# Kernel tuning notes

Hardware: AMD Instinct MI355X
Metric: run time of the kernel (lower is better)

Reference implementation:

```python
import jax, jax.numpy as jnp
import numpy as np

N = 100000   # nodes
E = 200000   # edges
G = 2000     # graphs
D = 300      # emb_dim
L = 5        # layers
FEAT = 512
MAX_DEGREE = 4
EPS = 1e-5


def setup_inputs() -> dict:
    key = jax.random.key(0)
    ks = jax.random.split(key, 24)
    atom_vocab = jnp.array([119, 3, 11, 9, 7, 4, 6, 2, 2])
    bond_vocab = jnp.array([4, 3, 2])  # keep type < 4 so self-loop type 4 is distinct
    x = jax.random.randint(ks[0], (N, 9), 0, 1 << 30) % atom_vocab
    edge_index = jax.random.randint(ks[1], (2, E), 0, N)
    edge_attr = jax.random.randint(ks[2], (E, 3), 0, 1 << 30) % bond_vocab
    edge_distance = jax.random.uniform(ks[3], (E,), dtype=jnp.float32) * 4.0
    batch = jnp.sort(jax.random.randint(ks[4], (N,), 0, G))
    nrm = lambda k, s, sc: (jax.random.normal(k, s, dtype=jnp.float32) * sc)
    return {
        "x": x, "edge_index": edge_index, "edge_attr": edge_attr,
        "edge_distance": edge_distance, "batch": batch,
        "atom_emb": nrm(ks[5], (9, 119, D), 0.1),
        "att_vec": nrm(ks[6], (D,), 1.0),
        "out_lin_w": nrm(ks[7], (D, D), 0.05), "out_lin_b": jnp.zeros((D,)),
        "g_means": jax.random.uniform(ks[8], (D,), minval=2.0, maxval=3.0),
        "g_stds": jax.random.uniform(ks[9], (D,), minval=1.0, maxval=1.5),
        "scale_param": jnp.full((MAX_DEGREE, D), np.log(0.1), dtype=jnp.float32),
        "edge_emb": nrm(ks[10], (L, 3, 5, D), 0.1),
        "mlp_w1": nrm(ks[11], (L, D, 2 * D), 0.05), "mlp_b1": jnp.zeros((L, 2 * D)),
        "mlp_w2": nrm(ks[12], (L, 2 * D, D), 0.05), "mlp_b2": jnp.zeros((L, D)),
        "bn_gamma": jnp.ones((L, D)), "bn_beta": jnp.zeros((L, D)),
        "feat_w": nrm(ks[13], (D, FEAT), 0.05), "feat_b": jnp.zeros((FEAT,)),
        "ol_w1": nrm(ks[14], (FEAT, FEAT), 0.05), "ol_b1": jnp.zeros((FEAT,)),
        "ol_w2": nrm(ks[15], (FEAT, FEAT // 2), 0.05), "ol_b2": jnp.zeros((FEAT // 2,)),
    }


def reference(x, edge_index, edge_attr, edge_distance, batch,
              atom_emb, att_vec, out_lin_w, out_lin_b, g_means, g_stds, scale_param,
              edge_emb, mlp_w1, mlp_b1, mlp_w2, mlp_b2, bn_gamma, bn_beta,
              feat_w, feat_b, ol_w1, ol_b1, ol_w2, ol_b2):
    src, dst = edge_index[0], edge_index[1]
    # node degree from incoming edges, clamped as in the torch code
    counts = jax.ops.segment_sum(jnp.ones((E,), jnp.int32), dst, num_segments=N)
    node_degree = jnp.clip(counts - 1, 0, MAX_DEGREE - 1)
    # GaussianLayer on edge distances -> [E, D]
    std = jnp.abs(g_stds) + 0.01
    a = (2.0 * 3.14159) ** 0.5
    z = (edge_distance[:, None] - g_means[None, :]) / std[None, :]
    g = jnp.exp(-0.5 * z * z) / (a * std[None, :])
    h_in = jax.ops.segment_sum(g, dst, num_segments=N)          # [N, D]
    h_in = jnp.exp(scale_param)[node_degree] * h_in             # ScaleDegreeLayer
    # AtomEncoderAttention: [N, 9, D] embeddings fused by softmax attention
    embs = atom_emb[jnp.arange(9)[None, :], x]                  # [N, 9, D]
    scores = jnp.einsum('nfd,d->nf', embs, att_vec)
    w = jax.nn.softmax(scores, axis=1)
    fused = jnp.einsum('nfd,nf->nd', embs, w)
    h = fused @ out_lin_w + out_lin_b + h_in
    # self-loop augmented edges (same for every layer)
    loop = jnp.arange(N)
    src_a = jnp.concatenate([src, loop])
    dst_a = jnp.concatenate([dst, loop])
    loop_attr = jnp.tile(jnp.array([[4, 0, 0]], edge_attr.dtype), (N, 1))
    attr_a = jnp.concatenate([edge_attr, loop_attr], axis=0)    # [E+N, 3]
    for l in range(L):
        e = (edge_emb[l, 0][attr_a[:, 0]] + edge_emb[l, 1][attr_a[:, 1]]
             + edge_emb[l, 2][attr_a[:, 2]])                     # [E+N, D]
        msg = h[src_a] + e
        agg = jax.ops.segment_sum(msg, dst_a, num_segments=N)
        h = jax.nn.relu(agg @ mlp_w1[l] + mlp_b1[l]) @ mlp_w2[l] + mlp_b2[l]
        mu = h.mean(axis=0)
        var = jnp.mean((h - mu) ** 2, axis=0)
        h = bn_gamma[l] * (h - mu) * jax.lax.rsqrt(var + EPS) + bn_beta[l]
        if l < L - 1:
            h = jax.nn.relu(h)
    # global mean pool
    sums = jax.ops.segment_sum(h, batch, num_segments=G)
    cnt = jax.ops.segment_sum(jnp.ones((N,), h.dtype), batch, num_segments=G)
    hg = sums / jnp.maximum(cnt, 1.0)[:, None]
    h_feat = hg @ feat_w + feat_b                                # [G, 512]
    out = jax.nn.relu(h_feat @ ol_w1 + ol_b1) @ ol_w2 + ol_b2    # [G, 256]
    return (h_feat, out)
```

## Files before the change

### kernel.cpp

```cpp
#include <hip/hip_runtime.h>
#include <hip/hip_bf16.h>


#define NN   100000
#define EE   200000
#define GG   2000
#define DD   300
#define D2   600
#define LL   5
#define FEATN 512
#define OUT2 256
#define ROWS_PER 256
#define RPB  48
#define MLP_LDS (RPB * 632 * 2)

typedef __hip_bfloat16 bf16;
typedef short vec8s __attribute__((ext_vector_type(8)));
typedef short vec4s __attribute__((ext_vector_type(4)));
typedef float vec4f __attribute__((ext_vector_type(4)));

__device__ __forceinline__ short f2bs(float v) {
    bf16 h = __float2bfloat16(v);
    return __builtin_bit_cast(short, h);
}
__device__ __forceinline__ float bs2f(short s) {
    unsigned u = ((unsigned)(unsigned short)s) << 16;
    return __builtin_bit_cast(float, u);
}

__global__ void k_pack(const float* __restrict__ src, short* __restrict__ dst,
                       int Ksrc, int Nsrc, int KT, int NPAD)
{
    int idx = blockIdx.x * 256 + threadIdx.x;
    int total = KT * NPAD * 32;
    if (idx >= total) return;
    int col = idx % NPAD;
    int tmp = idx / NPAD;
    int kk  = tmp % 32;
    int kt  = tmp / 32;
    int k = kt * 32 + kk;
    short v = 0;
    if (k < Ksrc && col < Nsrc) v = f2bs(src[(size_t)k * Nsrc + col]);
    dst[((size_t)kt * NPAD + col) * 32 + kk] = v;
}

__global__ void k_etab(const float* __restrict__ edge_emb, float* __restrict__ E)
{
    int i = blockIdx.x * 256 + threadIdx.x;
    if (i >= LL * 25 * DD) return;
    int d = i % DD;
    int t = i / DD;
    int c = t % 25;
    int l = t / 25;
    int a0 = (c == 24) ? 4 : (c / 6);
    int a1 = (c == 24) ? 0 : ((c % 6) / 2);
    int a2 = (c == 24) ? 0 : (c % 2);
    const float* e0 = edge_emb + (size_t)((l * 3 + 0) * 5) * DD;
    const float* e1 = edge_emb + (size_t)((l * 3 + 1) * 5) * DD;
    const float* e2 = edge_emb + (size_t)((l * 3 + 2) * 5) * DD;
    E[i] = e0[a0 * DD + d] + e1[a1 * DD + d] + e2[a2 * DD + d];
}

__global__ void k_repack(int* __restrict__ eidx, const int* __restrict__ src,
                         const int* __restrict__ attr)
{
    int i = blockIdx.x * 256 + threadIdx.x;
    if (i >= EE) return;
    int e = eidx[i];
    int c = attr[e * 3] * 6 + attr[e * 3 + 1] * 2 + attr[e * 3 + 2];
    eidx[i] = src[e] | (c << 17);
}

__global__ __launch_bounds__(512, 4) void k_mlp2(
    const short* __restrict__ Qb, const short* __restrict__ W1P,
    const float* __restrict__ b1, const short* __restrict__ W2P,
    const float* __restrict__ b2, void* __restrict__ Pout, int f16out,
    float* __restrict__ RS)
{
    extern __shared__ __align__(16) char smem_c[];
    short* Apan = (short*)smem_c;
    short (*Hl)[632] = (short(*)[632])smem_c;

    const int t = threadIdx.x;
    const int wv = t >> 6, lane = t & 63;
    const int m = lane & 15, quad = lane >> 4;
    const int rb = (int)blockIdx.x * RPB;
    const int rep = ((int)blockIdx.x & 31) * 600;

    {
        const short* qbase = Qb + (size_t)rb * 320;
#pragma unroll
        for (int i = 0; i < 4; i++) {
            int j = i * 8 + wv;
            if (j < 30) {
                int c   = j * 64 + lane;
                int c8  = c >> 3;
                int row = c8 / 5;
                int ch  = (c8 - row * 5) * 8 + (lane & 7);
                const short* src = qbase + (size_t)row * 320
                                 + (size_t)((ch ^ (row & 7)) * 8);
                __builtin_amdgcn_global_load_lds(
                    (const __attribute__((address_space(1))) unsigned int*)src,
                    (__attribute__((address_space(3))) unsigned int*)(smem_c + j * 1024),
                    16, 0, 0);
            }
        }
    }

    const int ql   = quad ^ (m & 3);
    const int eh   = (m >> 2) & 1;
    const int abE  = m * 320 + ql * 8 + eh * 32;
    const int abO  = m * 320 + ql * 8 + (1 - eh) * 32;

    vec4f acc1[3][5];
#pragma unroll
    for (int g = 0; g < 3; g++)
#pragma unroll
        for (int cf = 0; cf < 5; cf++) acc1[g][cf] = (vec4f)0.f;

    const short* w1b = W1P + ((size_t)(wv * 80 + m) * 32) + quad * 8;
    vec8s bcur[5], bnxt[5];
#pragma unroll
    for (int cf = 0; cf < 5; cf++) bcur[cf] = *(const vec8s*)(w1b + cf * 512);

    __syncthreads();

#pragma unroll
    for (int kt = 0; kt < 10; kt++) {
        if (kt < 9) {
            const short* wn = w1b + (size_t)(kt + 1) * 20480;
#pragma unroll
            for (int cf = 0; cf < 5; cf++) bnxt[cf] = *(const vec8s*)(wn + cf * 512);
        }
        const int base = (kt & 1) ? abO : abE;
        const int koff = (kt & ~1) * 32;
        vec8s af[3];
#pragma unroll
        for (int g = 0; g < 3; g++)
            af[g] = *(const vec8s*)(Apan + base + koff + g * 5120);
        __builtin_amdgcn_s_setprio(1);
#pragma unroll
        for (int cf = 0; cf < 5; cf++)
#pragma unroll
            for (int g = 0; g < 3; g++)
                acc1[g][cf] = __builtin_amdgcn_mfma_f32_16x16x32_bf16(
                    bcur[cf], af[g], acc1[g][cf], 0, 0, 0);
        __builtin_amdgcn_s_setprio(0);
#pragma unroll
        for (int cf = 0; cf < 5; cf++) bcur[cf] = bnxt[cf];
    }

    const short* w2b = W2P + ((size_t)(wv * 48 + m) * 32) + quad * 8;
    vec8s b2f[2][3];
#pragma unroll
    for (int cf = 0; cf < 3; cf++) {
        b2f[0][cf] = *(const vec8s*)(w2b + cf * 512);
        b2f[1][cf] = *(const vec8s*)(w2b + 12288 + cf * 512);
    }

    __syncthreads();

#pragma unroll
    for (int g = 0; g < 3; g++) {
#pragma unroll
        for (int cf = 0; cf < 5; cf++) {
            const int col0 = wv * 80 + cf * 16 + quad * 4;
            if (col0 < 600) {
                vec4f bv = *(const vec4f*)(b1 + col0);
                vec4s o;
#pragma unroll
                for (int r = 0; r < 4; r++)
                    o[r] = f2bs(fmaxf(acc1[g][cf][r] + bv[r], 0.f));
                *(vec4s*)&Hl[g * 16 + m][col0] = o;
            } else if (col0 < 608) {
                *(vec4s*)&Hl[g * 16 + m][col0] = (vec4s)0;
            }
        }
    }
    __syncthreads();

    {
        vec4f acc2[3][3];
#pragma unroll
        for (int g = 0; g < 3; g++)
#pragma unroll
            for (int cf = 0; cf < 3; cf++) acc2[g][cf] = (vec4f)0.f;

#pragma unroll
        for (int kt = 0; kt < 19; kt++) {
            vec8s ha[3];
#pragma unroll
            for (int g = 0; g < 3; g++)
                ha[g] = *(const vec8s*)&Hl[g * 16 + m][kt * 32 + quad * 8];
            __builtin_amdgcn_s_setprio(1);
#pragma unroll
            for (int cf = 0; cf < 3; cf++)
#pragma unroll
                for (int g = 0; g < 3; g++)
                    acc2[g][cf] = __builtin_amdgcn_mfma_f32_16x16x32_bf16(
                        ha[g], b2f[kt & 1][cf], acc2[g][cf], 0, 0, 0);
            __builtin_amdgcn_s_setprio(0);
            if (kt < 17) {
                const short* wn = w2b + (size_t)(kt + 2) * 12288;
#pragma unroll
                for (int cf = 0; cf < 3; cf++)
                    b2f[kt & 1][cf] = *(const vec8s*)(wn + cf * 512);
            }
        }

#pragma unroll
        for (int cf = 0; cf < 3; cf++) {
            int gc = wv * 48 + cf * 16 + m;
            bool ok = (gc < DD);
            float bv = ok ? b2[gc] : 0.f;
            float s = 0.f, q = 0.f;
#pragma unroll
            for (int g = 0; g < 3; g++) {
#pragma unroll
                for (int reg = 0; reg < 4; reg++) {
                    int row = rb + g * 16 + quad * 4 + reg;
                    bool vr = row < NN;
                    float v = acc2[g][cf][reg] + bv;
                    if (ok && vr) {
                        if (f16out)
                            ((short*)Pout)[(size_t)row * 300 + gc] = f2bs(v);
                        else
                            ((float*)Pout)[(size_t)row * DD + gc] = v;
                    }
                    if (vr) { s += v; q += v * v; }
                }
            }
            s += __shfl_xor(s, 16); s += __shfl_xor(s, 32);
            q += __shfl_xor(q, 16); q += __shfl_xor(q, 32);
            if (ok && quad == 0) {
                atomicAdd(&RS[rep + gc], s);
                atomicAdd(&RS[19200 + rep + gc], q);
            }
        }
    }
}

__global__ __launch_bounds__(256) void k_g1(
    const short* __restrict__ Qb, const short* __restrict__ WP,
    const float* __restrict__ bias, float* __restrict__ H)
{
    const int t = threadIdx.x;
    const int wv = t >> 6, lane = t & 63;
    const int m = lane & 15, quad = lane >> 4;
    const int rb = (int)blockIdx.x * 32;
    const short* arow0 = Qb + (size_t)(rb + m) * 320 + quad * 8;
    const short* arow1 = arow0 + (size_t)16 * 320;
    const short* wb0 = WP + ((size_t)(wv * 80 + m) * 32) + quad * 8;

    vec4f acc[2][5];
#pragma unroll
    for (int g = 0; g < 2; g++)
#pragma unroll
        for (int cf = 0; cf < 5; cf++) acc[g][cf] = (vec4f)0.f;

    vec8s af0 = *(const vec8s*)arow0;
    vec8s af1 = *(const vec8s*)arow1;
    vec8s bcur[5], bnxt[5];
#pragma unroll
    for (int cf = 0; cf < 5; cf++) bcur[cf] = *(const vec8s*)(wb0 + cf * 512);

#pragma unroll
    for (int kt = 0; kt < 10; kt++) {
        vec8s an0 = af0, an1 = af1;
        if (kt < 9) {
            an0 = *(const vec8s*)(arow0 + (kt + 1) * 32);
            an1 = *(const vec8s*)(arow1 + (kt + 1) * 32);
            const short* wn = wb0 + (size_t)(kt + 1) * 12288;
#pragma unroll
            for (int cf = 0; cf < 5; cf++) bnxt[cf] = *(const vec8s*)(wn + cf * 512);
        }
#pragma unroll
        for (int cf = 0; cf < 5; cf++) {
            acc[0][cf] = __builtin_amdgcn_mfma_f32_16x16x32_bf16(af0, bcur[cf], acc[0][cf], 0, 0, 0);
            acc[1][cf] = __builtin_amdgcn_mfma_f32_16x16x32_bf16(af1, bcur[cf], acc[1][cf], 0, 0, 0);
        }
        af0 = an0; af1 = an1;
#pragma unroll
        for (int cf = 0; cf < 5; cf++) bcur[cf] = bnxt[cf];
    }
#pragma unroll
    for (int cf = 0; cf < 5; cf++) {
        int gc = wv * 80 + cf * 16 + m;
        if (gc >= DD) continue;
        float bv = bias[gc];
#pragma unroll
        for (int g = 0; g < 2; g++)
#pragma unroll
            for (int reg = 0; reg < 4; reg++)
                H[(size_t)(rb + g * 16 + quad * 4 + reg) * DD + gc] = acc[g][cf][reg] + bv;
    }
}

__global__ void k_degree(const int* __restrict__ dst, int* __restrict__ deg) {
    int e = blockIdx.x * 256 + threadIdx.x;
    if (e < EE) atomicAdd(&deg[dst[e]], 1);
}

__global__ void k_scan1(const int* __restrict__ deg, int* __restrict__ off,
                        int* __restrict__ bsum)
{
    __shared__ int s[256];
    int i = blockIdx.x * 256 + threadIdx.x;
    int v = (i < NN) ? deg[i] : 0;
    s[threadIdx.x] = v;
    __syncthreads();
    for (int o = 1; o < 256; o <<= 1) {
        int tv = (threadIdx.x >= o) ? s[threadIdx.x - o] : 0;
        __syncthreads();
        s[threadIdx.x] += tv;
        __syncthreads();
    }
    if (i < NN) off[i] = s[threadIdx.x] - v;
    if (threadIdx.x == 255) bsum[blockIdx.x] = s[255];
}

__global__ void k_scan2(int* __restrict__ bsum, int* __restrict__ off, int nb) {
    if (threadIdx.x != 0 || blockIdx.x != 0) return;
    int run = 0;
    for (int b = 0; b < nb; b++) { int t = bsum[b]; bsum[b] = run; run += t; }
    off[NN] = run;
}

__global__ void k_scan3(int* __restrict__ off, const int* __restrict__ bsum,
                        int* __restrict__ curs)
{
    int i = blockIdx.x * 256 + threadIdx.x;
    if (i >= NN) return;
    int v = off[i] + bsum[i >> 8];
    off[i] = v;
    curs[i] = v;
}

__global__ void k_fill(const int* __restrict__ dst, int* __restrict__ curs,
                       int* __restrict__ eidx)
{
    int e = blockIdx.x * 256 + threadIdx.x;
    if (e >= EE) return;
    int pos = atomicAdd(&curs[dst[e]], 1);
    eidx[pos] = e;
}

__global__ __launch_bounds__(256) void k_embed(
    const int* __restrict__ x, const float* __restrict__ atom_emb,
    const float* __restrict__ att_vec, short* __restrict__ fusedb)
{
    int wave = threadIdx.x >> 6;
    int lane = threadIdx.x & 63;
    int n = blockIdx.x * 4 + wave;
    if (n >= NN) return;

    float att[5];
#pragma unroll
    for (int j = 0; j < 5; j++) {
        int d = lane + 64 * j;
        att[j] = (d < DD) ? att_vec[d] : 0.f;
    }
    float emb[9][5];
    float sc[9];
#pragma unroll
    for (int f = 0; f < 9; f++) {
        int idx = x[n * 9 + f];
        const float* p = atom_emb + (size_t)(f * 119 + idx) * DD;
        float partial = 0.f;
#pragma unroll
        for (int j = 0; j < 5; j++) {
            int d = lane + 64 * j;
            float v = (d < DD) ? p[d] : 0.f;
            emb[f][j] = v;
            partial += v * att[j];
        }
#pragma unroll
        for (int off = 32; off; off >>= 1) partial += __shfl_xor(partial, off, 64);
        sc[f] = partial;
    }
    float mx = sc[0];
#pragma unroll
    for (int f = 1; f < 9; f++) mx = fmaxf(mx, sc[f]);
    float s = 0.f;
#pragma unroll
    for (int f = 0; f < 9; f++) { sc[f] = __expf(sc[f] - mx); s += sc[f]; }
    float inv = 1.f / s;
#pragma unroll
    for (int j = 0; j < 5; j++) {
        int d = lane + 64 * j;
        float acc = 0.f;
        if (d < DD) {
#pragma unroll
            for (int f = 0; f < 9; f++) acc += emb[f][j] * sc[f];
            acc *= inv;
        }
        fusedb[(size_t)n * 320 + d] = (d < DD) ? f2bs(acc) : (short)0;
    }
}

__global__ __launch_bounds__(320) void k_gaussg(
    const int* __restrict__ off, const int* __restrict__ eidx,
    const float* __restrict__ dist, const float* __restrict__ g_means,
    const float* __restrict__ g_stds, const float* __restrict__ scale_p,
    float* __restrict__ H)
{
    int n = blockIdx.x;
    int d = threadIdx.x;
    if (d >= DD) return;
    int beg = off[n], end = off[n + 1];
    if (beg == end) return;
    float sd = fabsf(g_stds[d]) + 0.01f;
    float mean = g_means[d];
    float inv_asd = 1.f / (2.5066263f * sd);
    float sum = 0.f;
    for (int i = beg; i < end; i++) {
        float xv = dist[eidx[i]];
        float z = (xv - mean) / sd;
        sum += __expf(-0.5f * z * z) * inv_asd;
    }
    int deg = end - beg;
    int c = deg - 1; c = c < 0 ? 0 : (c > 3 ? 3 : c);
    H[(size_t)n * DD + d] += __expf(scale_p[c * DD + d]) * sum;
}

__global__ __launch_bounds__(320) void k_agg(
    const void* __restrict__ P, const int* __restrict__ off,
    const int* __restrict__ eidxp, const float* __restrict__ E,
    const float* __restrict__ scale, const float* __restrict__ shift,
    int apply, short* __restrict__ Qb)
{
    int tn = threadIdx.x / 160;
    int td = threadIdx.x - tn * 160;
    int n = blockIdx.x * 2 + tn;
    if (n >= NN) return;
    int d2 = td * 2;
    if (d2 >= DD) {
        *(short*)&Qb[(size_t)n * 320 + d2] = 0;
        Qb[(size_t)n * 320 + d2 + 1] = 0;
        return;
    }
    const float* Pf = (const float*)P;
    const short* Ph = (const short*)P;
    float scx = 1.f, scy = 1.f, shx = 0.f, shy = 0.f;
    if (apply) {
        float2 s2 = *(const float2*)(scale + d2);
        float2 h2 = *(const float2*)(shift + d2);
        scx = s2.x; scy = s2.y; shx = h2.x; shy = h2.y;
    }
    float ax, ay;
    if (apply) {
        short2 pv = *(const short2*)(Ph + (size_t)n * 300 + d2);
        ax = fmaxf(bs2f(pv.x) * scx + shx, 0.f);
        ay = fmaxf(bs2f(pv.y) * scy + shy, 0.f);
    } else {
        float2 self = *(const float2*)(Pf + (size_t)n * DD + d2);
        ax = self.x; ay = self.y;
    }
    float2 es = *(const float2*)(E + 24 * DD + d2);
    ax += es.x; ay += es.y;
    int beg = off[n], end = off[n + 1];
    if (apply) {
        for (int i = beg; i < end; i++) {
            int v = eidxp[i];
            int s = v & 131071;
            int c = v >> 17;
            short2 pv = *(const short2*)(Ph + (size_t)s * 300 + d2);
            float px = fmaxf(bs2f(pv.x) * scx + shx, 0.f);
            float py = fmaxf(bs2f(pv.y) * scy + shy, 0.f);
            float2 ev = *(const float2*)(E + c * DD + d2);
            ax += px + ev.x; ay += py + ev.y;
        }
    } else {
        for (int i = beg; i < end; i++) {
            int v = eidxp[i];
            int s = v & 131071;
            int c = v >> 17;
            float2 pv = *(const float2*)(Pf + (size_t)s * DD + d2);
            float2 ev = *(const float2*)(E + c * DD + d2);
            ax += pv.x + ev.x; ay += pv.y + ev.y;
        }
    }
    short2 o; o.x = f2bs(ax); o.y = f2bs(ay);
    *(short2*)&Qb[(size_t)n * 320 + d2] = o;
}

__global__ void k_bnprep(const float* __restrict__ RS, float* __restrict__ SC,
                         const float* __restrict__ gamma,
                         const float* __restrict__ beta)
{
    int d = threadIdx.x + blockIdx.x * 256;
    if (d >= DD) return;
    float s = 0.f, q = 0.f;
    for (int r = 0; r < 32; r++) {
        s += RS[r * 600 + d];
        q += RS[19200 + r * 600 + d];
    }
    float mu = s * (1.f / NN);
    float var = q * (1.f / NN) - mu * mu;
    var = fmaxf(var, 0.f);
    float sc = gamma[d] * rsqrtf(var + 1e-5f);
    SC[d] = sc;
    SC[600 + d] = beta[d] - mu * sc;
}

__global__ void k_count(const int* __restrict__ batch, float* __restrict__ cnt) {
    int n = blockIdx.x * 256 + threadIdx.x;
    if (n < NN) atomicAdd(&cnt[batch[n]], 1.0f);
}

__global__ __launch_bounds__(320) void k_pool(const float* __restrict__ H,
                                              const int* __restrict__ batch,
                                              float* __restrict__ HG)
{
    __shared__ int sb[ROWS_PER];
    int r0 = blockIdx.x * ROWS_PER;
    int rend = min(r0 + ROWS_PER, NN);
    for (int i = threadIdx.x; i < rend - r0; i += 320) sb[i] = batch[r0 + i];
    __syncthreads();
    int d = threadIdx.x;
    if (d >= DD) return;
    int cur = sb[0];
    float acc = 0.f;
    for (int r = r0; r < rend; r++) {
        int b = sb[r - r0];
        if (b != cur) { atomicAdd(&HG[(size_t)cur * DD + d], acc); acc = 0.f; cur = b; }
        acc += H[(size_t)r * DD + d];
    }
    atomicAdd(&HG[(size_t)cur * DD + d], acc);
}

__global__ void k_hgdiv(float* __restrict__ HG, const float* __restrict__ cnt,
                        const float* __restrict__ SC)
{
    int idx = blockIdx.x * 256 + threadIdx.x;
    if (idx >= GG * DD) return;
    int d = idx % DD;
    float mean = HG[idx] / fmaxf(cnt[idx / DD], 1.0f);
    HG[idx] = mean * SC[d] + SC[600 + d];
}

__global__ __launch_bounds__(256) void k_gemm(
    const float* __restrict__ A, const float* __restrict__ W,
    const float* __restrict__ bias, float* __restrict__ Cf,
    float* __restrict__ Cout, int M, int K, int Ncol, int relu)
{
    __shared__ float Ash[16][33];
    const int tx = threadIdx.x & 15;
    const int ty = threadIdx.x >> 4;
    const int rb = blockIdx.y * 16;
    const int col = blockIdx.x * 64 + tx * 4;

    float acc[4] = {0.f, 0.f, 0.f, 0.f};

    for (int k0 = 0; k0 < K; k0 += 32) {
        {
            int r  = threadIdx.x >> 4;
            int kk = (threadIdx.x & 15) * 2;
            int row = rb + r;
            float vx = 0.f, vy = 0.f;
            if (row < M) {
                const float* ap = A + (size_t)row * K + k0 + kk;
                if (k0 + kk + 1 < K) {
                    float2 v = *(const float2*)ap;
                    vx = v.x; vy = v.y;
                } else if (k0 + kk < K) {
                    vx = ap[0];
                }
            }
            Ash[r][kk]     = vx;
            Ash[r][kk + 1] = vy;
        }
        __syncthreads();

        const int kmax = (K - k0 < 32) ? (K - k0) : 32;
        const float* wp = W + (size_t)k0 * Ncol + col;
#pragma unroll 4
        for (int k = 0; k < kmax; k++) {
            float4 wv = *(const float4*)(wp + (size_t)k * Ncol);
            float a = Ash[ty][k];
            acc[0] += a * wv.x; acc[1] += a * wv.y;
            acc[2] += a * wv.z; acc[3] += a * wv.w;
        }
        __syncthreads();
    }

    int row = rb + ty;
    if (row < M) {
        float4 bv = *(const float4*)(bias + col);
        float4 o;
        o.x = acc[0] + bv.x; o.y = acc[1] + bv.y;
        o.z = acc[2] + bv.z; o.w = acc[3] + bv.w;
        if (relu) {
            o.x = fmaxf(o.x, 0.f); o.y = fmaxf(o.y, 0.f);
            o.z = fmaxf(o.z, 0.f); o.w = fmaxf(o.w, 0.f);
        }
        if (Cf)   *(float4*)(Cf   + (size_t)row * Ncol + col) = o;
        if (Cout) *(float4*)(Cout + (size_t)row * Ncol + col) = o;
    }
}

extern "C" void kernel_launch(void* const* d_in, const int* in_sizes, int n_in,
                              void* d_out, int out_size, void* d_ws, size_t ws_size,
                              hipStream_t stream)
{
    const int*   x          = (const int*)  d_in[0];
    const int*   edge_index = (const int*)  d_in[1];
    const int*   edge_attr  = (const int*)  d_in[2];
    const float* edge_dist  = (const float*)d_in[3];
    const int*   batch      = (const int*)  d_in[4];
    const float* atom_emb   = (const float*)d_in[5];
    const float* att_vec    = (const float*)d_in[6];
    const float* out_lin_w  = (const float*)d_in[7];
    const float* out_lin_b  = (const float*)d_in[8];
    const float* g_means    = (const float*)d_in[9];
    const float* g_stds     = (const float*)d_in[10];
    const float* scale_p    = (const float*)d_in[11];
    const float* edge_emb   = (const float*)d_in[12];
    const float* mlp_w1     = (const float*)d_in[13];
    const float* mlp_b1     = (const float*)d_in[14];
    const float* mlp_w2     = (const float*)d_in[15];
    const float* mlp_b2     = (const float*)d_in[16];
    const float* bn_gamma   = (const float*)d_in[17];
    const float* bn_beta    = (const float*)d_in[18];
    const float* feat_w     = (const float*)d_in[19];
    const float* feat_b     = (const float*)d_in[20];
    const float* ol_w1      = (const float*)d_in[21];
    const float* ol_b1      = (const float*)d_in[22];
    const float* ol_w2      = (const float*)d_in[23];
    const float* ol_b2      = (const float*)d_in[24];
    (void)in_sizes; (void)n_in; (void)out_size; (void)ws_size;

    const int* srcp = edge_index;
    const int* dstp = edge_index + EE;

    char* ws = (char*)d_ws;
    size_t off_b = 0;
    auto alloc = [&](size_t bytes) -> char* {
        char* p = ws + off_b;
        off_b += (bytes + 255) & ~(size_t)255;
        return p;
    };
    float* H     = (float*)alloc((size_t)NN * DD * 4 + 256);
    float* AGG   = (float*)alloc((size_t)NN * DD * 4 + 256);
    int*   DEG   = (int*)  alloc((size_t)NN * 4);
    float* CNT   = (float*)alloc(GG * 4);
    float* HG    = (float*)alloc((size_t)GG * DD * 4);
    float* HFEAT = (float*)alloc((size_t)GG * FEATN * 4);
    float* TMP   = (float*)alloc((size_t)GG * FEATN * 4);

    short* OLWP = (short*)HG;
    short* W1P  = OLWP + (size_t)10 * 384 * 32;
    short* W2P  = W1P + (size_t)LL * 10 * 640 * 32;
    char*  csr  = (char*)(W2P + (size_t)LL * 19 * 384 * 32);
    int*   OFF  = (int*)csr;
    int*   CURS = (int*)(csr + 400128);
    int*   EIDX = (int*)(csr + 800128);
    float* ETAB = (float*)(csr + 1600256);
    float* REPS = (float*)(csr + 1750272);
    float* SCL  = (float*)(csr + 2518528);
    int*   BSUM = (int*)CNT;

    float* outp = (float*)d_out;

    hipFuncSetAttribute((const void*)k_mlp2,
                        hipFuncAttributeMaxDynamicSharedMemorySize, MLP_LDS);

    k_pack<<<480, 256, 0, stream>>>(out_lin_w, OLWP, 300, 300, 10, 384);
    for (int l = 0; l < LL; l++) {
        k_pack<<<800, 256, 0, stream>>>(mlp_w1 + (size_t)l * DD * D2,
                                        W1P + (size_t)l * 10 * 640 * 32, DD, D2, 10, 640);
        k_pack<<<912, 256, 0, stream>>>(mlp_w2 + (size_t)l * D2 * DD,
                                        W2P + (size_t)l * 19 * 384 * 32, D2, DD, 19, 384);
    }
    k_etab<<<(LL * 25 * DD + 255) / 256, 256, 0, stream>>>(edge_emb, ETAB);
    hipMemsetAsync(REPS, 0, (size_t)LL * 2 * 32 * 600 * 4, stream);

    hipMemsetAsync(DEG, 0, (size_t)NN * 4, stream);
    k_degree<<<(EE + 255) / 256, 256, 0, stream>>>(dstp, DEG);
    k_scan1<<<391, 256, 0, stream>>>(DEG, OFF, BSUM);
    k_scan2<<<1, 64, 0, stream>>>(BSUM, OFF, 391);
    k_scan3<<<391, 256, 0, stream>>>(OFF, BSUM, CURS);
    k_fill<<<(EE + 255) / 256, 256, 0, stream>>>(dstp, CURS, EIDX);

    short* QB = (short*)AGG;
    k_embed<<<(NN + 3) / 4, 256, 0, stream>>>(x, atom_emb, att_vec, QB);
    k_g1<<<NN / 32, 256, 0, stream>>>(QB, OLWP, out_lin_b, H);
    k_gaussg<<<NN, 320, 0, stream>>>(OFF, EIDX, edge_dist, g_means, g_stds,
                                     scale_p, H);
    k_repack<<<(EE + 255) / 256, 256, 0, stream>>>(EIDX, srcp, edge_attr);

    for (int l = 0; l < LL; l++) {
        const float* sc = SCL + (size_t)(l - 1) * 1200;
        k_agg<<<(NN + 1) / 2, 320, 0, stream>>>(
            (const void*)H, OFF, EIDX, ETAB + (size_t)l * 25 * DD,
            l > 0 ? sc : SCL, l > 0 ? sc + 600 : SCL, l > 0 ? 1 : 0, QB);
        k_mlp2<<<(NN + RPB - 1) / RPB, 512, MLP_LDS, stream>>>(
            QB, W1P + (size_t)l * 10 * 640 * 32, mlp_b1 + (size_t)l * D2,
            W2P + (size_t)l * 19 * 384 * 32, mlp_b2 + (size_t)l * DD,
            (void*)H, (l < LL - 1) ? 1 : 0,
            REPS + (size_t)l * 38400);
        k_bnprep<<<2, 256, 0, stream>>>(REPS + (size_t)l * 38400,
                                        SCL + (size_t)l * 1200,
                                        bn_gamma + (size_t)l * DD,
                                        bn_beta + (size_t)l * DD);
    }

    hipMemsetAsync(CNT, 0, (size_t)GG * 4, stream);
    hipMemsetAsync(HG, 0, (size_t)GG * DD * 4, stream);
    k_count<<<(NN + 255) / 256, 256, 0, stream>>>(batch, CNT);
    k_pool<<<(NN + ROWS_PER - 1) / ROWS_PER, 320, 0, stream>>>(H, batch, HG);
    k_hgdiv<<<(GG * DD + 255) / 256, 256, 0, stream>>>(HG, CNT,
                                                       SCL + (size_t)4 * 1200);
    {
        dim3 grid((FEATN + 63) / 64, (GG + 15) / 16);
        k_gemm<<<grid, 256, 0, stream>>>(HG, feat_w, feat_b, HFEAT, outp,
                                         GG, DD, FEATN, 0);
    }
    {
        dim3 grid((FEATN + 63) / 64, (GG + 15) / 16);
        k_gemm<<<grid, 256, 0, stream>>>(HFEAT, ol_w1, ol_b1, TMP, nullptr,
                                         GG, FEATN, FEATN, 1);
    }
    {
        dim3 grid((OUT2 + 63) / 64, (GG + 15) / 16);
        k_gemm<<<grid, 256, 0, stream>>>(TMP, ol_w2, ol_b2, nullptr,
                                         outp + (size_t)GG * FEATN,
                                         GG, FEATN, OUT2, 0);
    }
}
```

Measured before the change: 2.046 ms.

## Parallelize block-sum scan, prefetch edge indices, fold node counting into pooling

The single-thread serial scan of 391 block sums is replaced by a 512-thread wavefront-shuffle scan. The gaussian and aggregation loops now prefetch the next edge index (software pipelining) to hide the dependent-load latency. Graph node counting moves into the pooling kernel, which removes one launch and its atomics. Each piece is small, and the prefetch adds a conditional load per iteration.

```diff
diff --git a/kernel.cpp b/kernel.cpp
--- a/kernel.cpp
+++ b/kernel.cpp
@@ -320,10 +320,29 @@
 }
 
 __global__ void k_scan2(int* __restrict__ bsum, int* __restrict__ off, int nb) {
-    if (threadIdx.x != 0 || blockIdx.x != 0) return;
-    int run = 0;
-    for (int b = 0; b < nb; b++) { int t = bsum[b]; bsum[b] = run; run += t; }
-    off[NN] = run;
+    __shared__ int ws[8];
+    int t = threadIdx.x;
+    int v = (t < nb) ? bsum[t] : 0;
+    int s = v;
+    for (int o = 1; o < 64; o <<= 1) {
+        int u = __shfl_up(s, o, 64);
+        if ((t & 63) >= o) s += u;
+    }
+    if ((t & 63) == 63) ws[t >> 6] = s;
+    __syncthreads();
+    if (t < 8) {
+        int a = ws[t];
+        for (int o = 1; o < 8; o <<= 1) {
+            int u = __shfl_up(a, o, 64);
+            if (t >= o) a += u;
+        }
+        ws[t] = a;
+    }
+    __syncthreads();
+    int base = (t >> 6) ? ws[(t >> 6) - 1] : 0;
+    int incl = s + base;
+    if (t < nb) bsum[t] = incl - v;
+    if (t == nb - 1) off[NN] = incl;
 }
 
 __global__ void k_scan3(int* __restrict__ off, const int* __restrict__ bsum,
@@ -413,10 +432,13 @@
     float mean = g_means[d];
     float inv_asd = 1.f / (2.5066263f * sd);
     float sum = 0.f;
+    float xv = dist[eidx[beg]];
     for (int i = beg; i < end; i++) {
-        float xv = dist[eidx[i]];
+        float xn = 0.f;
+        if (i + 1 < end) xn = dist[eidx[i + 1]];
         float z = (xv - mean) / sd;
         sum += __expf(-0.5f * z * z) * inv_asd;
+        xv = xn;
     }
     int deg = end - beg;
     int c = deg - 1; c = c < 0 ? 0 : (c > 3 ? 3 : c);
@@ -459,25 +481,31 @@
     float2 es = *(const float2*)(E + 24 * DD + d2);
     ax += es.x; ay += es.y;
     int beg = off[n], end = off[n + 1];
-    if (apply) {
-        for (int i = beg; i < end; i++) {
-            int v = eidxp[i];
-            int s = v & 131071;
-            int c = v >> 17;
-            short2 pv = *(const short2*)(Ph + (size_t)s * 300 + d2);
-            float px = fmaxf(bs2f(pv.x) * scx + shx, 0.f);
-            float py = fmaxf(bs2f(pv.y) * scy + shy, 0.f);
-            float2 ev = *(const float2*)(E + c * DD + d2);
-            ax += px + ev.x; ay += py + ev.y;
-        }
-    } else {
-        for (int i = beg; i < end; i++) {
-            int v = eidxp[i];
-            int s = v & 131071;
-            int c = v >> 17;
-            float2 pv = *(const float2*)(Pf + (size_t)s * DD + d2);
-            float2 ev = *(const float2*)(E + c * DD + d2);
-            ax += pv.x + ev.x; ay += pv.y + ev.y;
+    if (beg < end) {
+        int v = eidxp[beg];
+        if (apply) {
+            for (int i = beg; i < end; i++) {
+                int vn = 0;
+                if (i + 1 < end) vn = eidxp[i + 1];
+                int s = v & 131071;
+                int c = v >> 17;
+                short2 pv = *(const short2*)(Ph + (size_t)s * 300 + d2);
+                float2 ev = *(const float2*)(E + c * DD + d2);
+                ax += fmaxf(bs2f(pv.x) * scx + shx, 0.f) + ev.x;
+                ay += fmaxf(bs2f(pv.y) * scy + shy, 0.f) + ev.y;
+                v = vn;
+            }
+        } else {
+            for (int i = beg; i < end; i++) {
+                int vn = 0;
+                if (i + 1 < end) vn = eidxp[i + 1];
+                int s = v & 131071;
+                int c = v >> 17;
+                float2 pv = *(const float2*)(Pf + (size_t)s * DD + d2);
+                float2 ev = *(const float2*)(E + c * DD + d2);
+                ax += pv.x + ev.x; ay += pv.y + ev.y;
+                v = vn;
+            }
         }
     }
     short2 o; o.x = f2bs(ax); o.y = f2bs(ay);
@@ -503,14 +531,10 @@
     SC[600 + d] = beta[d] - mu * sc;
 }
 
-__global__ void k_count(const int* __restrict__ batch, float* __restrict__ cnt) {
-    int n = blockIdx.x * 256 + threadIdx.x;
-    if (n < NN) atomicAdd(&cnt[batch[n]], 1.0f);
-}
-
 __global__ __launch_bounds__(320) void k_pool(const float* __restrict__ H,
                                               const int* __restrict__ batch,
-                                              float* __restrict__ HG)
+                                              float* __restrict__ HG,
+                                              float* __restrict__ cnt)
 {
     __shared__ int sb[ROWS_PER];
     int r0 = blockIdx.x * ROWS_PER;
@@ -521,12 +545,19 @@
     if (d >= DD) return;
     int cur = sb[0];
     float acc = 0.f;
+    int run = 0;
     for (int r = r0; r < rend; r++) {
         int b = sb[r - r0];
-        if (b != cur) { atomicAdd(&HG[(size_t)cur * DD + d], acc); acc = 0.f; cur = b; }
+        if (b != cur) {
+            atomicAdd(&HG[(size_t)cur * DD + d], acc);
+            if (d == 0) atomicAdd(&cnt[cur], (float)run);
+            acc = 0.f; run = 0; cur = b;
+        }
         acc += H[(size_t)r * DD + d];
+        run++;
     }
     atomicAdd(&HG[(size_t)cur * DD + d], acc);
+    if (d == 0) atomicAdd(&cnt[cur], (float)run);
 }
 
 __global__ void k_hgdiv(float* __restrict__ HG, const float* __restrict__ cnt,
@@ -678,7 +709,7 @@
     hipMemsetAsync(DEG, 0, (size_t)NN * 4, stream);
     k_degree<<<(EE + 255) / 256, 256, 0, stream>>>(dstp, DEG);
     k_scan1<<<391, 256, 0, stream>>>(DEG, OFF, BSUM);
-    k_scan2<<<1, 64, 0, stream>>>(BSUM, OFF, 391);
+    k_scan2<<<1, 512, 0, stream>>>(BSUM, OFF, 391);
     k_scan3<<<391, 256, 0, stream>>>(OFF, BSUM, CURS);
     k_fill<<<(EE + 255) / 256, 256, 0, stream>>>(dstp, CURS, EIDX);
 
@@ -707,8 +738,7 @@
 
     hipMemsetAsync(CNT, 0, (size_t)GG * 4, stream);
     hipMemsetAsync(HG, 0, (size_t)GG * DD * 4, stream);
-    k_count<<<(NN + 255) / 256, 256, 0, stream>>>(batch, CNT);
-    k_pool<<<(NN + ROWS_PER - 1) / ROWS_PER, 320, 0, stream>>>(H, batch, HG);
+    k_pool<<<(NN + ROWS_PER - 1) / ROWS_PER, 320, 0, stream>>>(H, batch, HG, CNT);
     k_hgdiv<<<(GG * DD + 255) / 256, 256, 0, stream>>>(HG, CNT,
                                                        SCL + (size_t)4 * 1200);
     {
```

New measurement: 1.903 ms. 7.0% less time.
